# Kernel optimization log

Hardware: AMD Instinct MI355X
Metric: run time of the kernel (lower is better)

Reference implementation:

```python
import jax, jax.numpy as jnp
import numpy as np

NEG_INF = -1e9  # Keras uses a large negative for masked logits


def setup_inputs() -> dict:
    key = jax.random.key(0)
    k1, k2, k3, k4, k5 = jax.random.split(key, 5)
    B, Tq, Tv, D, U = 8, 128, 128, 512, 1024
    query = jax.random.normal(k1, (B, Tq, D), dtype=jnp.float32)
    value = jax.random.normal(k2, (B, Tv, D), dtype=jnp.float32)
    mask = jnp.ones((B, Tv), dtype=bool)
    # Dense(units, use_bias=False) kernels and AdditiveAttention scale vector
    W1 = jax.random.normal(k3, (D, U), dtype=jnp.float32) * (1.0 / np.sqrt(D))
    W2 = jax.random.normal(k4, (D, U), dtype=jnp.float32) * (1.0 / np.sqrt(D))
    scale = jax.random.normal(k5, (U,), dtype=jnp.float32) * (1.0 / np.sqrt(U))
    return {"query": query, "value": value, "mask": mask,
            "W1": W1, "W2": W2, "scale": scale}


def reference(query, value, mask, W1, W2, scale):
    # Projections (Dense, no bias)
    wq = jnp.einsum('btd,du->btu', query, W1)   # [B, Tq, U]
    wk = jnp.einsum('bsd,du->bsu', value, W2)   # [B, Tv, U]
    # Additive (Bahdanau) scores: sum_u scale_u * tanh(wq + wk)
    # Materializes [B, Tq, Tv, U] broadcast-add like Keras AdditiveAttention.
    scores = jnp.einsum('u,btsu->bts', scale,
                        jnp.tanh(wq[:, :, None, :] + wk[:, None, :, :]))
    # value mask over key axis (query_mask is all-ones in the source -> no-op)
    scores = jnp.where(mask[:, None, :], scores, NEG_INF)
    attn = jax.nn.softmax(scores, axis=-1)       # [B, Tq, Tv]
    context = jnp.einsum('bts,bsd->btd', attn, value)  # [B, Tq, D]
    return context, attn
```

## Files before the change

### kernel.cpp

```cpp
#include <hip/hip_runtime.h>

#define B_  8
#define TQ  128
#define TV  128
#define DIM 512
#define UU  1024
#define NSPLIT 8
#define NP  (B_ * TQ * TV)
#define C2  2.885390081777927f

typedef __attribute__((ext_vector_type(8))) short     short8;
typedef __attribute__((ext_vector_type(4))) float     f32x4;
typedef __attribute__((ext_vector_type(4))) unsigned short us4;

__device__ __forceinline__ unsigned short bf16_rtne(float x) {
    unsigned u = __float_as_uint(x);
    unsigned r = u + 0x7FFF + ((u >> 16) & 1);
    return (unsigned short)(r >> 16);
}
__device__ __forceinline__ float bf16_to_f(unsigned short h) {
    return __uint_as_float(((unsigned)h) << 16);
}

__global__ __launch_bounds__(256) void k_prep_a(
    const float* __restrict__ Q, const float* __restrict__ Vv,
    unsigned short* __restrict__ Ah, unsigned short* __restrict__ Al)
{
    int idx = blockIdx.x * 256 + threadIdx.x;
    int mat = idx >> 17;
    const float* src = mat ? Vv : Q;
    int off = (idx & 131071) * 4;
    float4 v = *(const float4*)&src[off];
    us4 h, l;
    h.x = bf16_rtne(v.x); l.x = bf16_rtne(v.x - bf16_to_f(h.x));
    h.y = bf16_rtne(v.y); l.y = bf16_rtne(v.y - bf16_to_f(h.y));
    h.z = bf16_rtne(v.z); l.z = bf16_rtne(v.z - bf16_to_f(h.z));
    h.w = bf16_rtne(v.w); l.w = bf16_rtne(v.w - bf16_to_f(h.w));
    *(us4*)&Ah[mat * 524288 + off] = h;
    *(us4*)&Al[mat * 524288 + off] = l;
}

__global__ __launch_bounds__(256) void k_prep_w(
    const float* __restrict__ W1, const float* __restrict__ W2,
    unsigned short* __restrict__ Wh, unsigned short* __restrict__ Wl)
{
    __shared__ float ts[32][36];
    const int t   = threadIdx.x;
    const int mat = blockIdx.z;
    const int n0  = blockIdx.x * 32;
    const int k0  = blockIdx.y * 32;
    const float* W = mat ? W2 : W1;

    int kk = t >> 3, n4 = (t & 7) * 4;
    float4 w = *(const float4*)&W[(k0 + kk) * UU + n0 + n4];
    ts[n4 + 0][kk] = w.x; ts[n4 + 1][kk] = w.y;
    ts[n4 + 2][kk] = w.z; ts[n4 + 3][kk] = w.w;
    __syncthreads();

    int nn = t >> 3, k4 = (t & 7) * 4;
    float4 v = *(const float4*)&ts[nn][k4];
    us4 h, l;
    h.x = bf16_rtne(v.x); l.x = bf16_rtne(v.x - bf16_to_f(h.x));
    h.y = bf16_rtne(v.y); l.y = bf16_rtne(v.y - bf16_to_f(h.y));
    h.z = bf16_rtne(v.z); l.z = bf16_rtne(v.z - bf16_to_f(h.z));
    h.w = bf16_rtne(v.w); l.w = bf16_rtne(v.w - bf16_to_f(h.w));
    unsigned off = mat * 524288 + (n0 + nn) * 512 + k0 + k4;
    *(us4*)&Wh[off] = h;
    *(us4*)&Wl[off] = l;
}

#define PK 40
__global__ __launch_bounds__(256) void k_proj(
    const unsigned short* __restrict__ Ah, const unsigned short* __restrict__ Al,
    const unsigned short* __restrict__ Bh, const unsigned short* __restrict__ Bl,
    float* __restrict__ Eq, float* __restrict__ Ek)
{
    __shared__ short sAh[64 * PK], sAl[64 * PK], sBh[64 * PK], sBl[64 * PK];

    const int tid  = threadIdx.x;
    const int wave = tid >> 6;
    const int lane = tid & 63;
    const int mat  = blockIdx.z;
    const int m0   = blockIdx.y * 64;
    const int n0   = blockIdx.x * 64;

    const unsigned mb = mat * 524288u;
    const int wm = (wave & 1) * 32;
    const int wn = (wave >> 1) * 32;

    const int sm = tid >> 2, sg = tid & 3;
    const unsigned short* gAh = Ah + mb + (m0 + sm) * 512 + sg * 8;
    const unsigned short* gAl = Al + mb + (m0 + sm) * 512 + sg * 8;
    const unsigned short* gBh = Bh + mb + (n0 + sm) * 512 + sg * 8;
    const unsigned short* gBl = Bl + mb + (n0 + sm) * 512 + sg * 8;
    const int sOff = sm * PK + sg * 8;

    const int fr = lane & 15, fq = lane >> 4;
    const int aOff0 = (wm + fr) * PK + fq * 8;
    const int aOff1 = (wm + 16 + fr) * PK + fq * 8;
    const int bOff0 = (wn + fr) * PK + fq * 8;
    const int bOff1 = (wn + 16 + fr) * PK + fq * 8;

    f32x4 acc00 = {0.f, 0.f, 0.f, 0.f};
    f32x4 acc01 = {0.f, 0.f, 0.f, 0.f};
    f32x4 acc10 = {0.f, 0.f, 0.f, 0.f};
    f32x4 acc11 = {0.f, 0.f, 0.f, 0.f};

    for (int kc = 0; kc < 16; ++kc) {
        int4 vah = *(const int4*)(gAh + kc * 32);
        int4 val = *(const int4*)(gAl + kc * 32);
        int4 vbh = *(const int4*)(gBh + kc * 32);
        int4 vbl = *(const int4*)(gBl + kc * 32);
        *(int4*)&sAh[sOff] = vah;
        *(int4*)&sAl[sOff] = val;
        *(int4*)&sBh[sOff] = vbh;
        *(int4*)&sBl[sOff] = vbl;
        __syncthreads();

        short8 a0h = *(const short8*)&sAh[aOff0];
        short8 a0l = *(const short8*)&sAl[aOff0];
        short8 a1h = *(const short8*)&sAh[aOff1];
        short8 a1l = *(const short8*)&sAl[aOff1];
        short8 b0h = *(const short8*)&sBh[bOff0];
        short8 b0l = *(const short8*)&sBl[bOff0];
        short8 b1h = *(const short8*)&sBh[bOff1];
        short8 b1l = *(const short8*)&sBl[bOff1];

        acc00 = __builtin_amdgcn_mfma_f32_16x16x32_bf16(a0h, b0h, acc00, 0, 0, 0);
        acc00 = __builtin_amdgcn_mfma_f32_16x16x32_bf16(a0h, b0l, acc00, 0, 0, 0);
        acc00 = __builtin_amdgcn_mfma_f32_16x16x32_bf16(a0l, b0h, acc00, 0, 0, 0);

        acc01 = __builtin_amdgcn_mfma_f32_16x16x32_bf16(a0h, b1h, acc01, 0, 0, 0);
        acc01 = __builtin_amdgcn_mfma_f32_16x16x32_bf16(a0h, b1l, acc01, 0, 0, 0);
        acc01 = __builtin_amdgcn_mfma_f32_16x16x32_bf16(a0l, b1h, acc01, 0, 0, 0);

        acc10 = __builtin_amdgcn_mfma_f32_16x16x32_bf16(a1h, b0h, acc10, 0, 0, 0);
        acc10 = __builtin_amdgcn_mfma_f32_16x16x32_bf16(a1h, b0l, acc10, 0, 0, 0);
        acc10 = __builtin_amdgcn_mfma_f32_16x16x32_bf16(a1l, b0h, acc10, 0, 0, 0);

        acc11 = __builtin_amdgcn_mfma_f32_16x16x32_bf16(a1h, b1h, acc11, 0, 0, 0);
        acc11 = __builtin_amdgcn_mfma_f32_16x16x32_bf16(a1h, b1l, acc11, 0, 0, 0);
        acc11 = __builtin_amdgcn_mfma_f32_16x16x32_bf16(a1l, b1h, acc11, 0, 0, 0);
        __syncthreads();
    }

    float* C = mat ? Ek : Eq;
    #pragma unroll
    for (int r = 0; r < 4; ++r) {
        int row0 = m0 + wm + fq * 4 + r;
        int row1 = row0 + 16;
        int col0 = n0 + wn + fr;
        C[row0 * UU + col0]      = __builtin_amdgcn_exp2f(C2 * acc00[r]);
        C[row0 * UU + col0 + 16] = __builtin_amdgcn_exp2f(C2 * acc01[r]);
        C[row1 * UU + col0]      = __builtin_amdgcn_exp2f(C2 * acc10[r]);
        C[row1 * UU + col0 + 16] = __builtin_amdgcn_exp2f(C2 * acc11[r]);
    }
}
#undef PK

__global__ __launch_bounds__(256) void k_scores(
    const float* __restrict__ Eq, const float* __restrict__ Ek,
    const float* __restrict__ scale, float* __restrict__ part)
{
    __shared__ float qs[32][132];
    __shared__ float ks[32][132];
    __shared__ float ss[128];

    const int tid = threadIdx.x;
    const int tx  = tid & 15;
    const int ty  = tid >> 4;
    const int b   = blockIdx.z & 7;
    const int us  = blockIdx.z >> 3;
    const int t0  = blockIdx.y * 32;
    const int s0  = blockIdx.x * 32;
    const int u0  = us * (UU / NSPLIT);

    {
        const int c  = (tid & 31) * 4;
        const int r0 = tid >> 5;
        #pragma unroll
        for (int i = 0; i < 4; ++i) {
            int r = r0 + i * 8;
            *(float4*)&qs[r][c] = *(const float4*)&Eq[(b * TQ + t0 + r) * UU + u0 + c];
            *(float4*)&ks[r][c] = *(const float4*)&Ek[(b * TV + s0 + r) * UU + u0 + c];
        }
        if (tid < 32)
            *(float4*)&ss[tid * 4] = *(const float4*)&scale[u0 + tid * 4];
    }
    __syncthreads();

    float a00 = 0.f, a01 = 0.f, a10 = 0.f, a11 = 0.f;

    #pragma unroll 4
    for (int u4 = 0; u4 < 32; ++u4) {
        float4 q0 = *(const float4*)&qs[ty][u4 * 4];
        float4 q1 = *(const float4*)&qs[ty + 16][u4 * 4];
        float4 k0 = *(const float4*)&ks[tx][u4 * 4];
        float4 k1 = *(const float4*)&ks[tx + 16][u4 * 4];
        float4 sv = *(const float4*)&ss[u4 * 4];

        #define PAIR(ACC, QV, KV)                                           \
        {                                                                   \
            float p1 = QV.x * KV.x, p2 = QV.y * KV.y;                       \
            float b1 = p1 + 1.f,   b2 = p2 + 1.f;                           \
            float n1 = fmaf(sv.y, b1, sv.x * b2);                           \
            ACC = fmaf(n1, __builtin_amdgcn_rcpf(b1 * b2), ACC);            \
            float p3 = QV.z * KV.z, p4 = QV.w * KV.w;                       \
            float b3 = p3 + 1.f,   b4 = p4 + 1.f;                           \
            float n2 = fmaf(sv.w, b3, sv.z * b4);                           \
            ACC = fmaf(n2, __builtin_amdgcn_rcpf(b3 * b4), ACC);            \
        }
        PAIR(a00, q0, k0)
        PAIR(a01, q0, k1)
        PAIR(a10, q1, k0)
        PAIR(a11, q1, k1)
        #undef PAIR
    }

    const int t = t0 + ty, s = s0 + tx;
    float* p = &part[us * NP + (b * TQ + t) * TV + s];
    p[0]            = a00;
    p[16]           = a01;
    p[16 * TV]      = a10;
    p[16 * TV + 16] = a11;
}

__global__ __launch_bounds__(256) void k_softmax(
    const float* __restrict__ part, const int* __restrict__ mask,
    float* __restrict__ attn)
{
    const int tid  = threadIdx.x;
    const int wave = tid >> 6;
    const int lane = tid & 63;
    const int row  = blockIdx.x * 4 + wave;
    const int b    = row >> 7;
    const int base = row * TV;

    float p0 = 0.f, p1 = 0.f;
    #pragma unroll
    for (int i = 0; i < NSPLIT; ++i) {
        p0 += part[i * NP + base + lane];
        p1 += part[i * NP + base + lane + 64];
    }
    float x0 = -2.f * p0, x1 = -2.f * p1;
    if (!mask[b * TV + lane])      x0 = -1e9f;
    if (!mask[b * TV + lane + 64]) x1 = -1e9f;

    float m = fmaxf(x0, x1);
    #pragma unroll
    for (int o = 32; o > 0; o >>= 1) m = fmaxf(m, __shfl_xor(m, o, 64));
    const float L2E = 1.4426950408889634f;
    float e0 = __builtin_amdgcn_exp2f((x0 - m) * L2E);
    float e1 = __builtin_amdgcn_exp2f((x1 - m) * L2E);
    float s = e0 + e1;
    #pragma unroll
    for (int o = 32; o > 0; o >>= 1) s += __shfl_xor(s, o, 64);
    float r = __builtin_amdgcn_rcpf(s);
    attn[base + lane]      = e0 * r;
    attn[base + lane + 64] = e1 * r;
}

__global__ __launch_bounds__(256) void k_context(
    const float* __restrict__ attn, const float* __restrict__ Vv,
    float* __restrict__ ctx)
{
    __shared__ float at[128][20];

    const int tid = threadIdx.x;
    const int b   = blockIdx.z;
    const int tt  = blockIdx.y;
    const int dc  = blockIdx.x;
    {
        int tl = tid & 15;
        int s0 = (tid >> 4) * 8;
        const float* src = &attn[(b * TQ + tt * 16 + tl) * TV + s0];
        float4 a0 = *(const float4*)src;
        float4 a1 = *(const float4*)(src + 4);
        at[s0 + 0][tl] = a0.x; at[s0 + 1][tl] = a0.y;
        at[s0 + 2][tl] = a0.z; at[s0 + 3][tl] = a0.w;
        at[s0 + 4][tl] = a1.x; at[s0 + 5][tl] = a1.y;
        at[s0 + 6][tl] = a1.z; at[s0 + 7][tl] = a1.w;
    }
    __syncthreads();

    const int d  = (tid & 127) + dc * 128;
    const int tg = tid >> 7;
    float acc[8] = {};
    const float* vp = &Vv[b * TV * DIM + d];
    for (int s = 0; s < TV; ++s) {
        float v = vp[s * DIM];
        float4 a0 = *(const float4*)&at[s][tg * 8];
        float4 a1 = *(const float4*)&at[s][tg * 8 + 4];
        acc[0] = fmaf(a0.x, v, acc[0]);
        acc[1] = fmaf(a0.y, v, acc[1]);
        acc[2] = fmaf(a0.z, v, acc[2]);
        acc[3] = fmaf(a0.w, v, acc[3]);
        acc[4] = fmaf(a1.x, v, acc[4]);
        acc[5] = fmaf(a1.y, v, acc[5]);
        acc[6] = fmaf(a1.z, v, acc[6]);
        acc[7] = fmaf(a1.w, v, acc[7]);
    }
    #pragma unroll
    for (int j = 0; j < 8; ++j) {
        int t = tt * 16 + tg * 8 + j;
        ctx[(b * TQ + t) * DIM + d] = acc[j];
    }
}

extern "C" void kernel_launch(void* const* d_in, const int* in_sizes, int n_in,
                              void* d_out, int out_size, void* d_ws, size_t ws_size,
                              hipStream_t stream)
{
    const float* query = (const float*)d_in[0];
    const float* value = (const float*)d_in[1];
    const int*   mask  = (const int*)d_in[2];
    const float* W1    = (const float*)d_in[3];
    const float* W2    = (const float*)d_in[4];
    const float* scale = (const float*)d_in[5];

    float* out  = (float*)d_out;
    float* ctx  = out;
    float* attn = out + B_ * TQ * DIM;

    float* Eq   = (float*)d_ws;
    float* Ek   = Eq + 1024 * 1024;
    float* part = Ek + 1024 * 1024;
    unsigned short* Ah = (unsigned short*)(part + NSPLIT * NP);
    unsigned short* Al = Ah + 2 * 1024 * 512;
    unsigned short* Wh = Al + 2 * 1024 * 512;
    unsigned short* Wl = Wh + 2 * 1024 * 512;

    hipLaunchKernelGGL(k_prep_a, dim3(1024),       dim3(256), 0, stream,
                       query, value, Ah, Al);
    hipLaunchKernelGGL(k_prep_w, dim3(32, 16, 2),  dim3(256), 0, stream,
                       W1, W2, Wh, Wl);
    hipLaunchKernelGGL(k_proj,   dim3(16, 16, 2),  dim3(256), 0, stream,
                       Ah, Al, Wh, Wl, Eq, Ek);
    hipLaunchKernelGGL(k_scores, dim3(4, 4, 8 * NSPLIT), dim3(256), 0, stream,
                       Eq, Ek, scale, part);
    hipLaunchKernelGGL(k_softmax, dim3(256),       dim3(256), 0, stream,
                       part, mask, attn);
    hipLaunchKernelGGL(k_context, dim3(4, 8, 8),   dim3(256), 0, stream,
                       attn, value, ctx);
}
```

Before: 117.5 us.

## Merge prep kernels, fuse softmax into context, double-buffer proj K loop

The two bf16 split-prep kernels are combined into one launch keyed on block index. The softmax kernel is folded into the context kernel, so each block recomputes the softmax for its 16 rows from the split partials and keeps attn in shared memory, and only dc==0 blocks write attn out. The projection GEMM now uses 64-wide K chunks with register prefetch of the next chunk during MFMA work, halving the barrier count. Together these cut two launches and an attn round-trip through global memory, at the cost of softmax being recomputed four times and more registers in the projection kernel.

```diff
diff --git a/kernel.cpp b/kernel.cpp
--- a/kernel.cpp
+++ b/kernel.cpp
@@ -22,60 +22,63 @@
     return __uint_as_float(((unsigned)h) << 16);
 }
 
-__global__ __launch_bounds__(256) void k_prep_a(
+__global__ __launch_bounds__(256) void k_prep(
     const float* __restrict__ Q, const float* __restrict__ Vv,
-    unsigned short* __restrict__ Ah, unsigned short* __restrict__ Al)
-{
-    int idx = blockIdx.x * 256 + threadIdx.x;
-    int mat = idx >> 17;
-    const float* src = mat ? Vv : Q;
-    int off = (idx & 131071) * 4;
-    float4 v = *(const float4*)&src[off];
-    us4 h, l;
-    h.x = bf16_rtne(v.x); l.x = bf16_rtne(v.x - bf16_to_f(h.x));
-    h.y = bf16_rtne(v.y); l.y = bf16_rtne(v.y - bf16_to_f(h.y));
-    h.z = bf16_rtne(v.z); l.z = bf16_rtne(v.z - bf16_to_f(h.z));
-    h.w = bf16_rtne(v.w); l.w = bf16_rtne(v.w - bf16_to_f(h.w));
-    *(us4*)&Ah[mat * 524288 + off] = h;
-    *(us4*)&Al[mat * 524288 + off] = l;
-}
-
-__global__ __launch_bounds__(256) void k_prep_w(
     const float* __restrict__ W1, const float* __restrict__ W2,
+    unsigned short* __restrict__ Ah, unsigned short* __restrict__ Al,
     unsigned short* __restrict__ Wh, unsigned short* __restrict__ Wl)
 {
     __shared__ float ts[32][36];
-    const int t   = threadIdx.x;
-    const int mat = blockIdx.z;
-    const int n0  = blockIdx.x * 32;
-    const int k0  = blockIdx.y * 32;
-    const float* W = mat ? W2 : W1;
-
-    int kk = t >> 3, n4 = (t & 7) * 4;
-    float4 w = *(const float4*)&W[(k0 + kk) * UU + n0 + n4];
-    ts[n4 + 0][kk] = w.x; ts[n4 + 1][kk] = w.y;
-    ts[n4 + 2][kk] = w.z; ts[n4 + 3][kk] = w.w;
-    __syncthreads();
-
-    int nn = t >> 3, k4 = (t & 7) * 4;
-    float4 v = *(const float4*)&ts[nn][k4];
-    us4 h, l;
-    h.x = bf16_rtne(v.x); l.x = bf16_rtne(v.x - bf16_to_f(h.x));
-    h.y = bf16_rtne(v.y); l.y = bf16_rtne(v.y - bf16_to_f(h.y));
-    h.z = bf16_rtne(v.z); l.z = bf16_rtne(v.z - bf16_to_f(h.z));
-    h.w = bf16_rtne(v.w); l.w = bf16_rtne(v.w - bf16_to_f(h.w));
-    unsigned off = mat * 524288 + (n0 + nn) * 512 + k0 + k4;
-    *(us4*)&Wh[off] = h;
-    *(us4*)&Wl[off] = l;
-}
-
-#define PK 40
+    const int bx = blockIdx.x;
+    const int t  = threadIdx.x;
+
+    if (bx < 1024) {
+        int idx = bx * 256 + t;
+        int mat = idx >> 17;
+        const float* src = mat ? Vv : Q;
+        int off = (idx & 131071) * 4;
+        float4 v = *(const float4*)&src[off];
+        us4 h, l;
+        h.x = bf16_rtne(v.x); l.x = bf16_rtne(v.x - bf16_to_f(h.x));
+        h.y = bf16_rtne(v.y); l.y = bf16_rtne(v.y - bf16_to_f(h.y));
+        h.z = bf16_rtne(v.z); l.z = bf16_rtne(v.z - bf16_to_f(h.z));
+        h.w = bf16_rtne(v.w); l.w = bf16_rtne(v.w - bf16_to_f(h.w));
+        *(us4*)&Ah[mat * 524288 + off] = h;
+        *(us4*)&Al[mat * 524288 + off] = l;
+    } else {
+        int b2   = bx - 1024;
+        int mat  = b2 >> 9;
+        int tile = b2 & 511;
+        int n0 = (tile & 31) * 32;
+        int k0 = (tile >> 5) * 32;
+        const float* W = mat ? W2 : W1;
+
+        int kk = t >> 3, n4 = (t & 7) * 4;
+        float4 w = *(const float4*)&W[(k0 + kk) * UU + n0 + n4];
+        ts[n4 + 0][kk] = w.x; ts[n4 + 1][kk] = w.y;
+        ts[n4 + 2][kk] = w.z; ts[n4 + 3][kk] = w.w;
+        __syncthreads();
+
+        int nn = t >> 3, k4 = (t & 7) * 4;
+        float4 v = *(const float4*)&ts[nn][k4];
+        us4 h, l;
+        h.x = bf16_rtne(v.x); l.x = bf16_rtne(v.x - bf16_to_f(h.x));
+        h.y = bf16_rtne(v.y); l.y = bf16_rtne(v.y - bf16_to_f(h.y));
+        h.z = bf16_rtne(v.z); l.z = bf16_rtne(v.z - bf16_to_f(h.z));
+        h.w = bf16_rtne(v.w); l.w = bf16_rtne(v.w - bf16_to_f(h.w));
+        unsigned off = mat * 524288 + (n0 + nn) * 512 + k0 + k4;
+        *(us4*)&Wh[off] = h;
+        *(us4*)&Wl[off] = l;
+    }
+}
+
+#define PKP 72
 __global__ __launch_bounds__(256) void k_proj(
     const unsigned short* __restrict__ Ah, const unsigned short* __restrict__ Al,
     const unsigned short* __restrict__ Bh, const unsigned short* __restrict__ Bl,
     float* __restrict__ Eq, float* __restrict__ Ek)
 {
-    __shared__ short sAh[64 * PK], sAl[64 * PK], sBh[64 * PK], sBl[64 * PK];
+    __shared__ short sAh[64 * PKP], sAl[64 * PKP], sBh[64 * PKP], sBl[64 * PKP];
 
     const int tid  = threadIdx.x;
     const int wave = tid >> 6;
@@ -89,60 +92,78 @@
     const int wn = (wave >> 1) * 32;
 
     const int sm = tid >> 2, sg = tid & 3;
-    const unsigned short* gAh = Ah + mb + (m0 + sm) * 512 + sg * 8;
-    const unsigned short* gAl = Al + mb + (m0 + sm) * 512 + sg * 8;
-    const unsigned short* gBh = Bh + mb + (n0 + sm) * 512 + sg * 8;
-    const unsigned short* gBl = Bl + mb + (n0 + sm) * 512 + sg * 8;
-    const int sOff = sm * PK + sg * 8;
+    const unsigned short* gAh = Ah + mb + (m0 + sm) * 512;
+    const unsigned short* gAl = Al + mb + (m0 + sm) * 512;
+    const unsigned short* gBh = Bh + mb + (n0 + sm) * 512;
+    const unsigned short* gBl = Bl + mb + (n0 + sm) * 512;
+    const int so0 = sm * PKP + sg * 8;
+    const int so1 = sm * PKP + 32 + sg * 8;
 
     const int fr = lane & 15, fq = lane >> 4;
-    const int aOff0 = (wm + fr) * PK + fq * 8;
-    const int aOff1 = (wm + 16 + fr) * PK + fq * 8;
-    const int bOff0 = (wn + fr) * PK + fq * 8;
-    const int bOff1 = (wn + 16 + fr) * PK + fq * 8;
+    const int aOff0 = (wm + fr) * PKP + fq * 8;
+    const int aOff1 = (wm + 16 + fr) * PKP + fq * 8;
+    const int bOff0 = (wn + fr) * PKP + fq * 8;
+    const int bOff1 = (wn + 16 + fr) * PKP + fq * 8;
 
     f32x4 acc00 = {0.f, 0.f, 0.f, 0.f};
     f32x4 acc01 = {0.f, 0.f, 0.f, 0.f};
     f32x4 acc10 = {0.f, 0.f, 0.f, 0.f};
     f32x4 acc11 = {0.f, 0.f, 0.f, 0.f};
 
-    for (int kc = 0; kc < 16; ++kc) {
-        int4 vah = *(const int4*)(gAh + kc * 32);
-        int4 val = *(const int4*)(gAl + kc * 32);
-        int4 vbh = *(const int4*)(gBh + kc * 32);
-        int4 vbl = *(const int4*)(gBl + kc * 32);
-        *(int4*)&sAh[sOff] = vah;
-        *(int4*)&sAl[sOff] = val;
-        *(int4*)&sBh[sOff] = vbh;
-        *(int4*)&sBl[sOff] = vbl;
+    int4 rAh0, rAh1, rAl0, rAl1, rBh0, rBh1, rBl0, rBl1;
+    #define LOADALL(K)                                                       \
+        rAh0 = *(const int4*)(gAh + (K) + sg * 8);                           \
+        rAh1 = *(const int4*)(gAh + (K) + 32 + sg * 8);                      \
+        rAl0 = *(const int4*)(gAl + (K) + sg * 8);                           \
+        rAl1 = *(const int4*)(gAl + (K) + 32 + sg * 8);                      \
+        rBh0 = *(const int4*)(gBh + (K) + sg * 8);                           \
+        rBh1 = *(const int4*)(gBh + (K) + 32 + sg * 8);                      \
+        rBl0 = *(const int4*)(gBl + (K) + sg * 8);                           \
+        rBl1 = *(const int4*)(gBl + (K) + 32 + sg * 8);
+
+    LOADALL(0)
+
+    #pragma unroll 1
+    for (int kc = 0; kc < 8; ++kc) {
+        *(int4*)&sAh[so0] = rAh0;  *(int4*)&sAh[so1] = rAh1;
+        *(int4*)&sAl[so0] = rAl0;  *(int4*)&sAl[so1] = rAl1;
+        *(int4*)&sBh[so0] = rBh0;  *(int4*)&sBh[so1] = rBh1;
+        *(int4*)&sBl[so0] = rBl0;  *(int4*)&sBl[so1] = rBl1;
         __syncthreads();
 
-        short8 a0h = *(const short8*)&sAh[aOff0];
-        short8 a0l = *(const short8*)&sAl[aOff0];
-        short8 a1h = *(const short8*)&sAh[aOff1];
-        short8 a1l = *(const short8*)&sAl[aOff1];
-        short8 b0h = *(const short8*)&sBh[bOff0];
-        short8 b0l = *(const short8*)&sBl[bOff0];
-        short8 b1h = *(const short8*)&sBh[bOff1];
-        short8 b1l = *(const short8*)&sBl[bOff1];
-
-        acc00 = __builtin_amdgcn_mfma_f32_16x16x32_bf16(a0h, b0h, acc00, 0, 0, 0);
-        acc00 = __builtin_amdgcn_mfma_f32_16x16x32_bf16(a0h, b0l, acc00, 0, 0, 0);
-        acc00 = __builtin_amdgcn_mfma_f32_16x16x32_bf16(a0l, b0h, acc00, 0, 0, 0);
-
-        acc01 = __builtin_amdgcn_mfma_f32_16x16x32_bf16(a0h, b1h, acc01, 0, 0, 0);
-        acc01 = __builtin_amdgcn_mfma_f32_16x16x32_bf16(a0h, b1l, acc01, 0, 0, 0);
-        acc01 = __builtin_amdgcn_mfma_f32_16x16x32_bf16(a0l, b1h, acc01, 0, 0, 0);
-
-        acc10 = __builtin_amdgcn_mfma_f32_16x16x32_bf16(a1h, b0h, acc10, 0, 0, 0);
-        acc10 = __builtin_amdgcn_mfma_f32_16x16x32_bf16(a1h, b0l, acc10, 0, 0, 0);
-        acc10 = __builtin_amdgcn_mfma_f32_16x16x32_bf16(a1l, b0h, acc10, 0, 0, 0);
-
-        acc11 = __builtin_amdgcn_mfma_f32_16x16x32_bf16(a1h, b1h, acc11, 0, 0, 0);
-        acc11 = __builtin_amdgcn_mfma_f32_16x16x32_bf16(a1h, b1l, acc11, 0, 0, 0);
-        acc11 = __builtin_amdgcn_mfma_f32_16x16x32_bf16(a1l, b1h, acc11, 0, 0, 0);
+        if (kc < 7) { LOADALL((kc + 1) * 64) }
+
+        #pragma unroll
+        for (int ks = 0; ks < 2; ++ks) {
+            const int o = ks * 32;
+            short8 a0h = *(const short8*)&sAh[aOff0 + o];
+            short8 a0l = *(const short8*)&sAl[aOff0 + o];
+            short8 a1h = *(const short8*)&sAh[aOff1 + o];
+            short8 a1l = *(const short8*)&sAl[aOff1 + o];
+            short8 b0h = *(const short8*)&sBh[bOff0 + o];
+            short8 b0l = *(const short8*)&sBl[bOff0 + o];
+            short8 b1h = *(const short8*)&sBh[bOff1 + o];
+            short8 b1l = *(const short8*)&sBl[bOff1 + o];
+
+            acc00 = __builtin_amdgcn_mfma_f32_16x16x32_bf16(a0h, b0h, acc00, 0, 0, 0);
+            acc00 = __builtin_amdgcn_mfma_f32_16x16x32_bf16(a0h, b0l, acc00, 0, 0, 0);
+            acc00 = __builtin_amdgcn_mfma_f32_16x16x32_bf16(a0l, b0h, acc00, 0, 0, 0);
+
+            acc01 = __builtin_amdgcn_mfma_f32_16x16x32_bf16(a0h, b1h, acc01, 0, 0, 0);
+            acc01 = __builtin_amdgcn_mfma_f32_16x16x32_bf16(a0h, b1l, acc01, 0, 0, 0);
+            acc01 = __builtin_amdgcn_mfma_f32_16x16x32_bf16(a0l, b1h, acc01, 0, 0, 0);
+
+            acc10 = __builtin_amdgcn_mfma_f32_16x16x32_bf16(a1h, b0h, acc10, 0, 0, 0);
+            acc10 = __builtin_amdgcn_mfma_f32_16x16x32_bf16(a1h, b0l, acc10, 0, 0, 0);
+            acc10 = __builtin_amdgcn_mfma_f32_16x16x32_bf16(a1l, b0h, acc10, 0, 0, 0);
+
+            acc11 = __builtin_amdgcn_mfma_f32_16x16x32_bf16(a1h, b1h, acc11, 0, 0, 0);
+            acc11 = __builtin_amdgcn_mfma_f32_16x16x32_bf16(a1h, b1l, acc11, 0, 0, 0);
+            acc11 = __builtin_amdgcn_mfma_f32_16x16x32_bf16(a1l, b1h, acc11, 0, 0, 0);
+        }
         __syncthreads();
     }
+    #undef LOADALL
 
     float* C = mat ? Ek : Eq;
     #pragma unroll
@@ -156,7 +177,7 @@
         C[row1 * UU + col0 + 16] = __builtin_amdgcn_exp2f(C2 * acc11[r]);
     }
 }
-#undef PK
+#undef PKP
 
 __global__ __launch_bounds__(256) void k_scores(
     const float* __restrict__ Eq, const float* __restrict__ Ek,
@@ -225,61 +246,52 @@
     p[16 * TV + 16] = a11;
 }
 
-__global__ __launch_bounds__(256) void k_softmax(
+__global__ __launch_bounds__(256) void k_ctx(
     const float* __restrict__ part, const int* __restrict__ mask,
-    float* __restrict__ attn)
-{
-    const int tid  = threadIdx.x;
-    const int wave = tid >> 6;
-    const int lane = tid & 63;
-    const int row  = blockIdx.x * 4 + wave;
-    const int b    = row >> 7;
-    const int base = row * TV;
-
-    float p0 = 0.f, p1 = 0.f;
-    #pragma unroll
-    for (int i = 0; i < NSPLIT; ++i) {
-        p0 += part[i * NP + base + lane];
-        p1 += part[i * NP + base + lane + 64];
-    }
-    float x0 = -2.f * p0, x1 = -2.f * p1;
-    if (!mask[b * TV + lane])      x0 = -1e9f;
-    if (!mask[b * TV + lane + 64]) x1 = -1e9f;
-
-    float m = fmaxf(x0, x1);
-    #pragma unroll
-    for (int o = 32; o > 0; o >>= 1) m = fmaxf(m, __shfl_xor(m, o, 64));
+    const float* __restrict__ Vv,
+    float* __restrict__ attn, float* __restrict__ ctx)
+{
+    __shared__ float at[128][20];
+
+    const int tid = threadIdx.x;
+    const int dc  = blockIdx.x;
+    const int tt  = blockIdx.y;
+    const int b   = blockIdx.z;
+    const int t0  = tt * 16;
+    const int rg  = tid >> 4;
+    const int ln  = tid & 15;
+    const int base = (b * TQ + t0 + rg) * TV;
+
+    float x[8];
+    #pragma unroll
+    for (int j = 0; j < 8; ++j) {
+        const int s = ln + 16 * j;
+        float p = 0.f;
+        #pragma unroll
+        for (int i = 0; i < NSPLIT; ++i) p += part[i * NP + base + s];
+        x[j] = mask[b * TV + s] ? -2.f * p : -1e9f;
+    }
+    float m = x[0];
+    #pragma unroll
+    for (int j = 1; j < 8; ++j) m = fmaxf(m, x[j]);
+    #pragma unroll
+    for (int o = 8; o > 0; o >>= 1) m = fmaxf(m, __shfl_xor(m, o, 64));
     const float L2E = 1.4426950408889634f;
-    float e0 = __builtin_amdgcn_exp2f((x0 - m) * L2E);
-    float e1 = __builtin_amdgcn_exp2f((x1 - m) * L2E);
-    float s = e0 + e1;
-    #pragma unroll
-    for (int o = 32; o > 0; o >>= 1) s += __shfl_xor(s, o, 64);
-    float r = __builtin_amdgcn_rcpf(s);
-    attn[base + lane]      = e0 * r;
-    attn[base + lane + 64] = e1 * r;
-}
-
-__global__ __launch_bounds__(256) void k_context(
-    const float* __restrict__ attn, const float* __restrict__ Vv,
-    float* __restrict__ ctx)
-{
-    __shared__ float at[128][20];
-
-    const int tid = threadIdx.x;
-    const int b   = blockIdx.z;
-    const int tt  = blockIdx.y;
-    const int dc  = blockIdx.x;
-    {
-        int tl = tid & 15;
-        int s0 = (tid >> 4) * 8;
-        const float* src = &attn[(b * TQ + tt * 16 + tl) * TV + s0];
-        float4 a0 = *(const float4*)src;
-        float4 a1 = *(const float4*)(src + 4);
-        at[s0 + 0][tl] = a0.x; at[s0 + 1][tl] = a0.y;
-        at[s0 + 2][tl] = a0.z; at[s0 + 3][tl] = a0.w;
-        at[s0 + 4][tl] = a1.x; at[s0 + 5][tl] = a1.y;
-        at[s0 + 6][tl] = a1.z; at[s0 + 7][tl] = a1.w;
+    float e[8];
+    float sum = 0.f;
+    #pragma unroll
+    for (int j = 0; j < 8; ++j) {
+        e[j] = __builtin_amdgcn_exp2f((x[j] - m) * L2E);
+        sum += e[j];
+    }
+    #pragma unroll
+    for (int o = 8; o > 0; o >>= 1) sum += __shfl_xor(sum, o, 64);
+    const float r = __builtin_amdgcn_rcpf(sum);
+    #pragma unroll
+    for (int j = 0; j < 8; ++j) {
+        const float a = e[j] * r;
+        at[ln + 16 * j][rg] = a;
+        if (dc == 0) attn[base + ln + 16 * j] = a;
     }
     __syncthreads();
 
@@ -302,7 +314,7 @@
     }
     #pragma unroll
     for (int j = 0; j < 8; ++j) {
-        int t = tt * 16 + tg * 8 + j;
+        int t = t0 + tg * 8 + j;
         ctx[(b * TQ + t) * DIM + d] = acc[j];
     }
 }
@@ -330,16 +342,12 @@
     unsigned short* Wh = Al + 2 * 1024 * 512;
     unsigned short* Wl = Wh + 2 * 1024 * 512;
 
-    hipLaunchKernelGGL(k_prep_a, dim3(1024),       dim3(256), 0, stream,
-                       query, value, Ah, Al);
-    hipLaunchKernelGGL(k_prep_w, dim3(32, 16, 2),  dim3(256), 0, stream,
-                       W1, W2, Wh, Wl);
-    hipLaunchKernelGGL(k_proj,   dim3(16, 16, 2),  dim3(256), 0, stream,
+    hipLaunchKernelGGL(k_prep,   dim3(2048),            dim3(256), 0, stream,
+                       query, value, W1, W2, Ah, Al, Wh, Wl);
+    hipLaunchKernelGGL(k_proj,   dim3(16, 16, 2),       dim3(256), 0, stream,
                        Ah, Al, Wh, Wl, Eq, Ek);
     hipLaunchKernelGGL(k_scores, dim3(4, 4, 8 * NSPLIT), dim3(256), 0, stream,
                        Eq, Ek, scale, part);
-    hipLaunchKernelGGL(k_softmax, dim3(256),       dim3(256), 0, stream,
-                       part, mask, attn);
-    hipLaunchKernelGGL(k_context, dim3(4, 8, 8),   dim3(256), 0, stream,
-                       attn, value, ctx);
-}
+    hipLaunchKernelGGL(k_ctx,    dim3(4, 8, 8),         dim3(256), 0, stream,
+                       part, mask, value, attn, ctx);
+}
```

Result: faster. 112.9 us (-3.9%).
